# Kernel optimization log

Hardware: AMD Instinct MI355X
Metric: run time of the kernel (lower is better)

The kernel has to match this reference:

```python
import jax, jax.numpy as jnp
import numpy as np

D_MODEL = 768
N_HEADS = 12
D_HEAD = 64
WINDOW = 32
LOOK_BACK = 1
PAD_VALUE = 0
IGNORE = -1000000.0
BS = 2
SEQ = 1024  # multiple of WINDOW so autopad is a no-op


def setup_inputs() -> dict:
    key = jax.random.key(0)
    k0, k1, k2, k3, k4 = jax.random.split(key, 5)
    x = jax.random.normal(k0, (BS, SEQ, D_MODEL), dtype=jnp.float32)
    W_abcde = jax.random.normal(k1, (D_MODEL, 5 * N_HEADS * D_HEAD), dtype=jnp.float32) * (1.0 / np.sqrt(D_MODEL))
    b_abcde = jax.random.normal(k2, (5 * N_HEADS * D_HEAD,), dtype=jnp.float32) * 0.02
    W_O = jax.random.normal(k3, (N_HEADS * D_HEAD, D_MODEL), dtype=jnp.float32) * (1.0 / np.sqrt(N_HEADS * D_HEAD))
    b_O = jax.random.normal(k4, (D_MODEL,), dtype=jnp.float32) * 0.02
    return dict(x=x, W_abcde=W_abcde, b_abcde=b_abcde, W_O=W_O, b_O=b_O)


def _look_around(t, backward=LOOK_BACK, pad_value=0):
    # t: (B, n_windows, window, ...). Pad along the windows axis, then
    # concatenate [prev_window, current_window] along the within-window axis.
    nw = t.shape[1]
    pad = [(0, 0)] * t.ndim
    pad[1] = (backward, 0)
    tp = jnp.pad(t, pad, constant_values=pad_value)
    return jnp.concatenate([tp[:, i:i + nw] for i in range(backward + 1)], axis=2)


def reference(x, W_abcde, b_abcde, W_O, b_O):
    bs, ts, _ = x.shape
    nw = ts // WINDOW
    B = bs * N_HEADS

    abcde = x @ W_abcde + b_abcde                       # (bs, ts, 5*h*d)
    abcde = abcde.reshape(bs, ts, 5, N_HEADS, D_HEAD)
    abcde = jnp.transpose(abcde, (2, 0, 3, 1, 4))       # (5, bs, h, ts, d)
    abcde = abcde.reshape(5, B, nw, WINDOW, D_HEAD)     # windowed
    a, b, c, d, e = abcde[0], abcde[1], abcde[2], abcde[3], abcde[4]

    # position ids per window, and their look-around version (pad_value = cfg.pad_value)
    seq = jnp.arange(ts, dtype=jnp.int32).reshape(1, nw, WINDOW)      # (1, nw, w)
    bb_t = _look_around(seq, LOOK_BACK, PAD_VALUE)                    # (1, nw, 2w)
    qi = seq[..., :, None, None]    # query position  (n axis)
    kj = bb_t[..., None, :, None]   # a-token position (m axis)
    lk = bb_t[..., None, None, :]   # b-token position (l axis)
    # masked unless: t_b <= t_query AND t_a < t_b
    mask = (qi < lk) | (lk <= kj)   # (1, nw, w, 2w, 2w)

    la_a = _look_around(a)
    la_b = _look_around(b)
    la_d = _look_around(d)
    la_e = _look_around(e)

    # triple-interaction scores: (B, nw, w, 2w, 2w)
    attn = jnp.einsum('xnid,xnjd,xnkd->xnijk', c, la_a, la_b)
    # mask causal-invalid entries, and (as in original) exact zeros (padding dots)
    attn = jnp.where(mask | (attn == 0.0), IGNORE, attn)
    attn = attn / D_HEAD
    shp = attn.shape
    score = jax.nn.softmax(attn.reshape(shp[0], shp[1], shp[2], -1), axis=-1).reshape(shp)

    # dual value combine: D at the a-position (m), E at the b-position (l)
    z = jnp.einsum('xnijk,xnjd->xnid', score, la_d) \
        + jnp.einsum('xnijk,xnkd->xnid', score, la_e)

    z = z.reshape(bs, N_HEADS, nw, WINDOW, D_HEAD)
    z = jnp.transpose(z, (0, 2, 3, 1, 4)).reshape(bs, ts, N_HEADS * D_HEAD)
    return z @ W_O + b_O
```

## Files before the change

kernel.cpp:

```cpp
#include <hip/hip_runtime.h>
#include <math.h>
#include <stdint.h>

#define NH     12
#define DH     64
#define WIN    32
#define SEQL   1024
#define BSZ    2
#define NW     (SEQL / WIN)
#define DMODEL 768
#define NCOL   (5 * NH * DH)

typedef __attribute__((ext_vector_type(4))) float f32x4;
typedef __attribute__((ext_vector_type(8))) short bf16x8;
typedef unsigned short u16;

static __device__ __forceinline__ u16 f2bf(float f) {
  union { float f; unsigned u; } v; v.f = f;
  unsigned r = v.u + 0x7fffu + ((v.u >> 16) & 1u);
  return (u16)(r >> 16);
}
static __device__ __forceinline__ float bf2f(u16 u) {
  union { unsigned u; float f; } v; v.u = ((unsigned)u) << 16;
  return v.f;
}
static __device__ __forceinline__ unsigned cvt_pk_bf16(float lo, float hi) {
  unsigned p;
  asm("v_cvt_pk_bf16_f32 %0, %1, %2" : "=v"(p) : "v"(lo), "v"(hi));
  return p;
}

typedef const __attribute__((address_space(1))) unsigned int* as1_cu32;
typedef __attribute__((address_space(3))) unsigned int* as3_u32;
static __device__ __forceinline__ void gload_lds16(const void* g, void* l) {
  __builtin_amdgcn_global_load_lds(
      reinterpret_cast<as1_cu32>(reinterpret_cast<uintptr_t>(g)),
      reinterpret_cast<as3_u32>(reinterpret_cast<uintptr_t>(l)), 16, 0, 0);
}

__global__ __launch_bounds__(256)
void prep_kernel(const float* __restrict__ x, const float* __restrict__ W,
                 const float* __restrict__ WO, u16* __restrict__ xb,
                 u16* __restrict__ Wt, u16* __restrict__ WOt) {
  __shared__ u16 tile[64][68];
  const int bid = blockIdx.x;
  const int tid = threadIdx.x;

  if (bid < 1536) {
    const int i = bid * 256 + tid;
    const float4 v = reinterpret_cast<const float4*>(x)[i];
    ushort4 o;
    o.x = f2bf(v.x); o.y = f2bf(v.y); o.z = f2bf(v.z); o.w = f2bf(v.w);
    reinterpret_cast<ushort4*>(xb)[i] = o;
    return;
  }

  const float* S; u16* D; int K, N, n0, k0;
  if (bid < 2256) {
    const int b = bid - 1536;
    S = W; D = Wt; K = DMODEL; N = NCOL;
    n0 = (b % 60) * 64; k0 = (b / 60) * 64;
  } else {
    const int b = bid - 2256;
    S = WO; D = WOt; K = DMODEL; N = NH * DH;
    n0 = (b % 12) * 64; k0 = (b / 12) * 64;
  }
#pragma unroll
  for (int pass = 0; pass < 4; ++pass) {
    const int r = pass * 16 + (tid >> 4);
    const int c = (tid & 15) << 2;
    const float4 v = *reinterpret_cast<const float4*>(&S[(size_t)(k0 + r) * N + n0 + c]);
    tile[c + 0][r] = f2bf(v.x); tile[c + 1][r] = f2bf(v.y);
    tile[c + 2][r] = f2bf(v.z); tile[c + 3][r] = f2bf(v.w);
  }
  __syncthreads();
#pragma unroll
  for (int pass = 0; pass < 4; ++pass) {
    const int rn = pass * 16 + (tid >> 4);
    const int ck = (tid & 15) << 2;
    ushort4 o;
    o.x = tile[rn][ck + 0]; o.y = tile[rn][ck + 1];
    o.z = tile[rn][ck + 2]; o.w = tile[rn][ck + 3];
    *reinterpret_cast<ushort4*>(&D[(size_t)(n0 + rn) * K + k0 + ck]) = o;
  }
}

template<int BM, int BN, int WAVES_M, int WAVES_N, bool OUT_BF16>
__global__ __launch_bounds__(256)
void gemm_mfma_kernel(const u16* __restrict__ A, const u16* __restrict__ Bt,
                      const float* __restrict__ bias, void* __restrict__ Cout,
                      int M, int N, int K) {
  constexpr int BK = 64;
  constexpr int MT = BM / (16 * WAVES_M);
  constexpr int NT = BN / (16 * WAVES_N);
  constexpr int CHA = BM / 8;
  constexpr int CHB = BN / 8;
  __shared__ __align__(16) u16 As[BM * BK];
  __shared__ __align__(16) u16 Bs[BN * BK];

  const int tid  = threadIdx.x;
  const int w    = tid >> 6;
  const int lane = tid & 63;
  const int m16  = lane & 15;
  const int g    = lane >> 4;
  const int wr   = w / WAVES_N;
  const int wc   = w % WAVES_N;
  const int bm   = blockIdx.y * BM;
  const int bn   = blockIdx.x * BN;

  const int srow   = lane >> 3;
  const int srcCol = ((lane & 7) ^ srow) << 3;

  f32x4 acc[MT][NT];
#pragma unroll
  for (int i = 0; i < MT; ++i)
#pragma unroll
    for (int j = 0; j < NT; ++j) {
      f32x4 z = {0.f, 0.f, 0.f, 0.f};
      acc[i][j] = z;
    }

  for (int k0 = 0; k0 < K; k0 += BK) {
#pragma unroll
    for (int c = 0; c < CHA / 4; ++c) {
      const int ch = w * (CHA / 4) + c;
      const int r  = ch * 8 + srow;
      gload_lds16(A + (size_t)(bm + r) * K + k0 + srcCol, As + ch * 512);
    }
#pragma unroll
    for (int c = 0; c < CHB / 4; ++c) {
      const int ch = w * (CHB / 4) + c;
      const int r  = ch * 8 + srow;
      gload_lds16(Bt + (size_t)(bn + r) * K + k0 + srcCol, Bs + ch * 512);
    }
    __syncthreads();

#pragma unroll
    for (int kk = 0; kk < 2; ++kk) {
      const int cs = (((kk << 2) + g) ^ (m16 & 7)) << 3;
      bf16x8 af[MT], bf[NT];
#pragma unroll
      for (int i = 0; i < MT; ++i) {
        const int r = wr * (16 * MT) + i * 16 + m16;
        af[i] = *reinterpret_cast<const bf16x8*>(&As[r * 64 + cs]);
      }
#pragma unroll
      for (int j = 0; j < NT; ++j) {
        const int r = wc * (16 * NT) + j * 16 + m16;
        bf[j] = *reinterpret_cast<const bf16x8*>(&Bs[r * 64 + cs]);
      }
#pragma unroll
      for (int i = 0; i < MT; ++i)
#pragma unroll
        for (int j = 0; j < NT; ++j)
          acc[i][j] = __builtin_amdgcn_mfma_f32_16x16x32_bf16(af[i], bf[j], acc[i][j], 0, 0, 0);
    }
    __syncthreads();
  }

#pragma unroll
  for (int i = 0; i < MT; ++i) {
#pragma unroll
    for (int j = 0; j < NT; ++j) {
      const int col = bn + wc * 16 * NT + j * 16 + m16;
      const float bcol = bias[col];
#pragma unroll
      for (int rr = 0; rr < 4; ++rr) {
        const int row = bm + wr * 16 * MT + i * 16 + g * 4 + rr;
        const float v = acc[i][j][rr] + bcol;
        if (OUT_BF16)
          reinterpret_cast<u16*>(Cout)[(size_t)row * N + col] = f2bf(v);
        else
          reinterpret_cast<float*>(Cout)[(size_t)row * N + col] = v;
      }
    }
  }
}

__global__ __launch_bounds__(512, 3)
void attn_mfma_kernel(const u16* __restrict__ Y, u16* __restrict__ Z) {
  __shared__ __align__(16) u16 DET[64][136];
  __shared__ __align__(16) u16 RQ[32][136];
  __shared__ float tot_lds[32];

  const int n  = blockIdx.x;
  const int bh = blockIdx.y;
  const int bi = bh / NH;
  const int h  = bh % NH;
  const int tid  = threadIdx.x;
  const int wv   = tid >> 6;
  const int lane = tid & 63;
  const int m16  = lane & 15;
  const int g    = lane >> 4;
  const int g4   = g << 2;
  const u16* Yb = Y + (size_t)bi * SEQL * NCOL;

  {
    const int j  = lane;
    const int r8 = wv * 8;
    const int t  = n * WIN - WIN + j;
    if (t >= 0) {
      const bf16x8 dv = *reinterpret_cast<const bf16x8*>(
          Yb + (size_t)t * NCOL + (3 * NH + h) * DH + r8);
      const bf16x8 ev = *reinterpret_cast<const bf16x8*>(
          Yb + (size_t)t * NCOL + (4 * NH + h) * DH + r8);
#pragma unroll
      for (int e = 0; e < 8; ++e) {
        DET[r8 + e][j]      = (u16)dv[e];
        DET[r8 + e][64 + j] = (u16)ev[e];
      }
    } else {
#pragma unroll
      for (int e = 0; e < 8; ++e) {
        DET[r8 + e][j] = 0;
        DET[r8 + e][64 + j] = 0;
      }
    }
  }

  bf16x8 afr[4][2], bfrb[4][2];
#pragma unroll
  for (int jt = 0; jt < 4; ++jt) {
    const int t = n * WIN - WIN + jt * 16 + m16;
#pragma unroll
    for (int ks = 0; ks < 2; ++ks) {
      if (n == 0 && jt < 2) {
        bf16x8 z = {0, 0, 0, 0, 0, 0, 0, 0};
        afr[jt][ks] = z;
        bfrb[jt][ks] = z;
      } else {
        afr[jt][ks] = *reinterpret_cast<const bf16x8*>(
            Yb + (size_t)t * NCOL + h * DH + ks * 32 + g * 8);
        bfrb[jt][ks] = *reinterpret_cast<const bf16x8*>(
            Yb + (size_t)t * NCOL + (NH + h) * DH + ks * 32 + g * 8);
      }
    }
  }

  const float K2 = 0.015625f * 1.44269504088896341f;
  const u16* crow_base = Yb + (size_t)(n * WIN) * NCOL + (2 * NH + h) * DH;

  for (int ii = 0; ii < 4; ++ii) {
    const int i = wv * 4 + ii;
    const u16* cp = crow_base + (size_t)i * NCOL;

    bf16x8 craw[2];
    craw[0] = *reinterpret_cast<const bf16x8*>(cp + g * 8);
    craw[1] = *reinterpret_cast<const bf16x8*>(cp + 32 + g * 8);
    float cf[2][8];
#pragma unroll
    for (int ks = 0; ks < 2; ++ks)
#pragma unroll
      for (int e = 0; e < 8; ++e) cf[ks][e] = bf2f((u16)craw[ks][e]) * K2;

    f32x4 acc[4][4];
#pragma unroll
    for (int kt = 0; kt < 4; ++kt)
#pragma unroll
      for (int jt = 0; jt <= kt; ++jt) {
        f32x4 z = {0.f, 0.f, 0.f, 0.f};
        acc[jt][kt] = z;
      }

#pragma unroll
    for (int ks = 0; ks < 2; ++ks) {
#pragma unroll
      for (int kt = 0; kt < 4; ++kt) {
        bf16x8 vf;
#pragma unroll
        for (int e = 0; e < 8; e += 2) {
          const float lo = bf2f((u16)bfrb[kt][ks][e])     * cf[ks][e];
          const float hi = bf2f((u16)bfrb[kt][ks][e + 1]) * cf[ks][e + 1];
          reinterpret_cast<unsigned*>(&vf)[e >> 1] = cvt_pk_bf16(lo, hi);
        }
#pragma unroll
        for (int jt = 0; jt <= kt; ++jt)
          acc[jt][kt] = __builtin_amdgcn_mfma_f32_16x16x32_bf16(afr[jt][ks], vf, acc[jt][kt], 0, 0, 0);
      }
    }

    float rp[16], qp[4];
#pragma unroll
    for (int u = 0; u < 16; ++u) rp[u] = 0.f;
#pragma unroll
    for (int u = 0; u < 4; ++u) qp[u] = 0.f;
#pragma unroll
    for (int kt = 0; kt < 4; ++kt) {
      const bool ck = (kt < 2) ? true : (kt * 16 + m16 <= i + 32);
#pragma unroll
      for (int jt = 0; jt <= kt; ++jt) {
        const bool rok = (jt >= 2) || (n > 0);
        const bool base = ck && rok;
#pragma unroll
        for (int r = 0; r < 4; ++r) {
          const bool valid = (jt == kt) ? (base && (m16 > g4 + r)) : base;
          const float e = valid ? __builtin_amdgcn_exp2f(acc[jt][kt][r]) : 0.f;
          rp[jt * 4 + r] += e;
          qp[kt] += e;
        }
      }
    }

    float rsel, qsel, tp;
    if (n == 0 && i == 0) {
      rsel = 1.f; qsel = 1.f; tp = 64.f;
    } else {
      float tin = (qp[0] + qp[1]) + (qp[2] + qp[3]);
#pragma unroll
      for (int off = 1; off <= 32; off <<= 1) tin += __shfl_xor(tin, off);
      tp = tin;

      float v8[8];
      {
        const bool b = (m16 & 1) != 0;
#pragma unroll
        for (int t2 = 0; t2 < 8; ++t2) {
          const float keep = b ? rp[2 * t2 + 1] : rp[2 * t2];
          const float send = b ? rp[2 * t2] : rp[2 * t2 + 1];
          v8[t2] = keep + __shfl_xor(send, 1);
        }
      }
      float v4s[4];
      {
        const bool b = (m16 & 2) != 0;
#pragma unroll
        for (int t2 = 0; t2 < 4; ++t2) {
          const float keep = b ? v8[2 * t2 + 1] : v8[2 * t2];
          const float send = b ? v8[2 * t2] : v8[2 * t2 + 1];
          v4s[t2] = keep + __shfl_xor(send, 2);
        }
      }
      float v2s[2];
      {
        const bool b = (m16 & 4) != 0;
#pragma unroll
        for (int t2 = 0; t2 < 2; ++t2) {
          const float keep = b ? v4s[2 * t2 + 1] : v4s[2 * t2];
          const float send = b ? v4s[2 * t2] : v4s[2 * t2 + 1];
          v2s[t2] = keep + __shfl_xor(send, 4);
        }
      }
      {
        const bool b = (m16 & 8) != 0;
        const float keep = b ? v2s[1] : v2s[0];
        const float send = b ? v2s[0] : v2s[1];
        rsel = keep + __shfl_xor(send, 8);
      }
      float q2[2];
      {
        const bool b = (g & 1) != 0;
#pragma unroll
        for (int t2 = 0; t2 < 2; ++t2) {
          const float keep = b ? qp[2 * t2 + 1] : qp[2 * t2];
          const float send = b ? qp[2 * t2] : qp[2 * t2 + 1];
          q2[t2] = keep + __shfl_xor(send, 16);
        }
      }
      {
        const bool b = (g & 2) != 0;
        const float keep = b ? q2[1] : q2[0];
        const float send = b ? q2[0] : q2[1];
        qsel = keep + __shfl_xor(send, 32);
      }
    }

    RQ[i][(m16 >> 2) * 16 + g4 + (m16 & 3)] = f2bf(rsel);
    RQ[i][64 + g * 16 + m16] = f2bf(qsel);
    if (lane == 0) tot_lds[i] = tp;
  }

  __syncthreads();

  const int mt = wv >> 2;
  const int nt = wv & 3;
  f32x4 zac = {0.f, 0.f, 0.f, 0.f};
#pragma unroll
  for (int kq = 0; kq < 4; ++kq) {
    const bf16x8 bf = *reinterpret_cast<const bf16x8*>(&DET[nt * 16 + m16][kq * 32 + g * 8]);
    const bf16x8 af = *reinterpret_cast<const bf16x8*>(&RQ[mt * 16 + m16][kq * 32 + g * 8]);
    zac = __builtin_amdgcn_mfma_f32_16x16x32_bf16(af, bf, zac, 0, 0, 0);
  }
#pragma unroll
  for (int r = 0; r < 4; ++r) {
    const int i = mt * 16 + g4 + r;
    const int d = nt * 16 + m16;
    const float inv = __builtin_amdgcn_rcpf(tot_lds[i]);
    Z[((size_t)bi * SEQL + n * WIN + i) * (NH * DH) + h * DH + d] =
        f2bf(zac[r] * inv);
  }
}

extern "C" void kernel_launch(void* const* d_in, const int* in_sizes, int n_in,
                              void* d_out, int out_size, void* d_ws, size_t ws_size,
                              hipStream_t stream) {
  const float* x        = (const float*)d_in[0];
  const float* W_abcde  = (const float*)d_in[1];
  const float* b_abcde  = (const float*)d_in[2];
  const float* W_O      = (const float*)d_in[3];
  const float* b_O      = (const float*)d_in[4];
  float* out = (float*)d_out;

  const int M = BSZ * SEQL;

  u16* Yb  = (u16*)d_ws;
  u16* xb  = Yb  + (size_t)M * NCOL;
  u16* Wt  = xb  + (size_t)M * DMODEL;
  u16* WOt = Wt  + (size_t)NCOL * DMODEL;
  u16* Zb  = WOt + (size_t)(NH * DH) * DMODEL;

  prep_kernel<<<2400, 256, 0, stream>>>(x, W_abcde, W_O, xb, Wt, WOt);

  gemm_mfma_kernel<128, 128, 2, 2, true><<<dim3(NCOL / 128, M / 128), 256, 0, stream>>>(
      xb, Wt, b_abcde, Yb, M, NCOL, DMODEL);

  attn_mfma_kernel<<<dim3(NW, BSZ * NH), 512, 0, stream>>>(Yb, Zb);

  gemm_mfma_kernel<64, 64, 2, 2, false><<<dim3((NH * DH) / 64, M / 64), 256, 0, stream>>>(
      Zb, WOt, b_O, out, M, DMODEL, NH * DH);
}
```

Measured before the change: 146.2 us.

## Double-buffer GEMM LDS tiles and prefetch next query row in attention

The GEMM kernel now uses two LDS buffers per operand, so the global-to-LDS load of the next K tile is issued before the MFMAs on the current tile and overlaps with them. One of the two barriers per iteration is dropped. In the attention kernel the c-row load for the next query is issued one iteration early, and the per-column exp sum becomes a tree reduction to shorten the dependency chain. The cost is doubled LDS use in the GEMM, which may lower occupancy. The single barrier left per iteration must be enough to keep the buffer being overwritten safe from waves still reading it.

```diff
diff --git a/kernel.cpp b/kernel.cpp
--- a/kernel.cpp
+++ b/kernel.cpp
@@ -95,8 +95,8 @@
   constexpr int NT = BN / (16 * WAVES_N);
   constexpr int CHA = BM / 8;
   constexpr int CHB = BN / 8;
-  __shared__ __align__(16) u16 As[BM * BK];
-  __shared__ __align__(16) u16 Bs[BN * BK];
+  __shared__ __align__(16) u16 As[2][BM * BK];
+  __shared__ __align__(16) u16 Bs[2][BN * BK];
 
   const int tid  = threadIdx.x;
   const int w    = tid >> 6;
@@ -111,6 +111,21 @@
   const int srow   = lane >> 3;
   const int srcCol = ((lane & 7) ^ srow) << 3;
 
+  auto stage = [&](int buf, int k0) {
+#pragma unroll
+    for (int c = 0; c < CHA / 4; ++c) {
+      const int ch = w * (CHA / 4) + c;
+      const int r  = ch * 8 + srow;
+      gload_lds16(A + (size_t)(bm + r) * K + k0 + srcCol, &As[buf][ch * 512]);
+    }
+#pragma unroll
+    for (int c = 0; c < CHB / 4; ++c) {
+      const int ch = w * (CHB / 4) + c;
+      const int r  = ch * 8 + srow;
+      gload_lds16(Bt + (size_t)(bn + r) * K + k0 + srcCol, &Bs[buf][ch * 512]);
+    }
+  };
+
   f32x4 acc[MT][NT];
 #pragma unroll
   for (int i = 0; i < MT; ++i)
@@ -120,20 +135,13 @@
       acc[i][j] = z;
     }
 
+  stage(0, 0);
+  __syncthreads();
+
+  int cur = 0;
   for (int k0 = 0; k0 < K; k0 += BK) {
-#pragma unroll
-    for (int c = 0; c < CHA / 4; ++c) {
-      const int ch = w * (CHA / 4) + c;
-      const int r  = ch * 8 + srow;
-      gload_lds16(A + (size_t)(bm + r) * K + k0 + srcCol, As + ch * 512);
-    }
-#pragma unroll
-    for (int c = 0; c < CHB / 4; ++c) {
-      const int ch = w * (CHB / 4) + c;
-      const int r  = ch * 8 + srow;
-      gload_lds16(Bt + (size_t)(bn + r) * K + k0 + srcCol, Bs + ch * 512);
-    }
-    __syncthreads();
+    const int nk = k0 + BK;
+    if (nk < K) stage(cur ^ 1, nk);
 
 #pragma unroll
     for (int kk = 0; kk < 2; ++kk) {
@@ -142,12 +150,12 @@
 #pragma unroll
       for (int i = 0; i < MT; ++i) {
         const int r = wr * (16 * MT) + i * 16 + m16;
-        af[i] = *reinterpret_cast<const bf16x8*>(&As[r * 64 + cs]);
+        af[i] = *reinterpret_cast<const bf16x8*>(&As[cur][r * 64 + cs]);
       }
 #pragma unroll
       for (int j = 0; j < NT; ++j) {
         const int r = wc * (16 * NT) + j * 16 + m16;
-        bf[j] = *reinterpret_cast<const bf16x8*>(&Bs[r * 64 + cs]);
+        bf[j] = *reinterpret_cast<const bf16x8*>(&Bs[cur][r * 64 + cs]);
       }
 #pragma unroll
       for (int i = 0; i < MT; ++i)
@@ -156,6 +164,7 @@
           acc[i][j] = __builtin_amdgcn_mfma_f32_16x16x32_bf16(af[i], bf[j], acc[i][j], 0, 0, 0);
     }
     __syncthreads();
+    cur ^= 1;
   }
 
 #pragma unroll
@@ -240,18 +249,25 @@
   const float K2 = 0.015625f * 1.44269504088896341f;
   const u16* crow_base = Yb + (size_t)(n * WIN) * NCOL + (2 * NH + h) * DH;
 
+  bf16x8 craw0 = *reinterpret_cast<const bf16x8*>(
+      crow_base + (size_t)(wv * 4) * NCOL + g * 8);
+  bf16x8 craw1 = *reinterpret_cast<const bf16x8*>(
+      crow_base + (size_t)(wv * 4) * NCOL + 32 + g * 8);
+
   for (int ii = 0; ii < 4; ++ii) {
     const int i = wv * 4 + ii;
-    const u16* cp = crow_base + (size_t)i * NCOL;
-
-    bf16x8 craw[2];
-    craw[0] = *reinterpret_cast<const bf16x8*>(cp + g * 8);
-    craw[1] = *reinterpret_cast<const bf16x8*>(cp + 32 + g * 8);
+
     float cf[2][8];
 #pragma unroll
-    for (int ks = 0; ks < 2; ++ks)
-#pragma unroll
-      for (int e = 0; e < 8; ++e) cf[ks][e] = bf2f((u16)craw[ks][e]) * K2;
+    for (int e = 0; e < 8; ++e) {
+      cf[0][e] = bf2f((u16)craw0[e]) * K2;
+      cf[1][e] = bf2f((u16)craw1[e]) * K2;
+    }
+    if (ii < 3) {
+      const u16* cpn = crow_base + (size_t)(i + 1) * NCOL;
+      craw0 = *reinterpret_cast<const bf16x8*>(cpn + g * 8);
+      craw1 = *reinterpret_cast<const bf16x8*>(cpn + 32 + g * 8);
+    }
 
     f32x4 acc[4][4];
 #pragma unroll
@@ -291,13 +307,14 @@
       for (int jt = 0; jt <= kt; ++jt) {
         const bool rok = (jt >= 2) || (n > 0);
         const bool base = ck && rok;
+        float ev[4];
 #pragma unroll
         for (int r = 0; r < 4; ++r) {
           const bool valid = (jt == kt) ? (base && (m16 > g4 + r)) : base;
-          const float e = valid ? __builtin_amdgcn_exp2f(acc[jt][kt][r]) : 0.f;
-          rp[jt * 4 + r] += e;
-          qp[kt] += e;
-        }
+          ev[r] = valid ? __builtin_amdgcn_exp2f(acc[jt][kt][r]) : 0.f;
+          rp[jt * 4 + r] += ev[r];
+        }
+        qp[kt] += (ev[0] + ev[1]) + (ev[2] + ev[3]);
       }
     }
 
```

Measured after the change: 150.4 us. +2.9%, slower.
